# Kernel tuning notes

Measured on AMD Instinct MI355X. Metric: run time of the kernel, lower is better.

The kernel has to match this reference:

```python
import jax, jax.numpy as jnp
import numpy as np

NEG_SLOPE = 0.2  # PyG GATConv default negative_slope


def gat_conv(x, edge_index, W, a_src, a_dst, bias, heads, out_ch, concat):
    """PyG-style GATConv (eval mode, add_self_loops=True).
    x: [N, F_in], edge_index: [2, E] (row 0 = src, row 1 = dst).
    """
    N = x.shape[0]
    loop = jnp.arange(N, dtype=edge_index.dtype)
    src = jnp.concatenate([edge_index[0], loop])  # [E+N]
    dst = jnp.concatenate([edge_index[1], loop])

    h = (x @ W).reshape(N, heads, out_ch)            # [N, H, C]
    alpha_s = jnp.einsum('nhc,hc->nh', h, a_src)     # [N, H]
    alpha_d = jnp.einsum('nhc,hc->nh', h, a_dst)

    e = jax.nn.leaky_relu(alpha_s[src] + alpha_d[dst], NEG_SLOPE)  # [E+N, H]
    # softmax over incoming edges per destination node (numerically stable)
    m = jax.ops.segment_max(e, dst, num_segments=N)                # [N, H]
    ex = jnp.exp(e - m[dst])
    denom = jax.ops.segment_sum(ex, dst, num_segments=N)
    alpha = ex / (denom[dst] + 1e-16)                              # [E+N, H]

    msg = h[src] * alpha[:, :, None]                               # [E+N, H, C]
    out = jax.ops.segment_sum(msg, dst, num_segments=N)            # [N, H, C]
    out = out.reshape(N, heads * out_ch) if concat else out.mean(axis=1)
    return out + bias


def setup_inputs() -> dict:
    key = jax.random.key(0)
    ks = jax.random.split(key, 10)
    N, F_in, H, C1, LAT, E = 10000, 2000, 10, 128, 64, 150000
    hid = H * C1  # 1280
    x = jax.random.normal(ks[0], (N, F_in), dtype=jnp.float32)
    edge_index = jax.random.randint(ks[1], (2, E), 0, N, dtype=jnp.int64)
    # layer 1 params (glorot-ish scaling)
    W1 = jax.random.normal(ks[2], (F_in, H * C1), dtype=jnp.float32) * (1.0 / np.sqrt(F_in))
    a_src1 = jax.random.normal(ks[3], (H, C1), dtype=jnp.float32) * 0.1
    a_dst1 = jax.random.normal(ks[4], (H, C1), dtype=jnp.float32) * 0.1
    b1 = jnp.zeros((hid,), dtype=jnp.float32)
    # layer 2 params
    W2 = jax.random.normal(ks[5], (hid, H * LAT), dtype=jnp.float32) * (1.0 / np.sqrt(hid))
    a_src2 = jax.random.normal(ks[6], (H, LAT), dtype=jnp.float32) * 0.1
    a_dst2 = jax.random.normal(ks[7], (H, LAT), dtype=jnp.float32) * 0.1
    b2 = jnp.zeros((LAT,), dtype=jnp.float32)
    return {"x": x, "edge_index": edge_index,
            "W1": W1, "a_src1": a_src1, "a_dst1": a_dst1, "b1": b1,
            "W2": W2, "a_src2": a_src2, "a_dst2": a_dst2, "b2": b2}


def reference(x, edge_index, W1, a_src1, a_dst1, b1, W2, a_src2, a_dst2, b2):
    H, C1, LAT = 10, 128, 64
    h1 = gat_conv(x, edge_index, W1, a_src1, a_dst1, b1, H, C1, concat=True)
    h1 = jax.nn.relu(h1)
    h2 = gat_conv(h1, edge_index, W2, a_src2, a_dst2, b2, H, LAT, concat=False)
    return jax.nn.relu(h2)
```

## Files before the change

kernel.cpp:

```cpp
#include <hip/hip_runtime.h>

#define NN    10000
#define FIN   2000
#define NH    10
#define C1    128
#define C2    64
#define HC1   1280
#define HC2   640
#define MP    10240
#define K1P   2016

typedef _Float16 f16x8 __attribute__((ext_vector_type(8)));
typedef _Float16 f16x4 __attribute__((ext_vector_type(4)));
typedef _Float16 f16x2 __attribute__((ext_vector_type(2)));
typedef float    f32x4 __attribute__((ext_vector_type(4)));

__device__ __forceinline__ float leaky(float x) { return x > 0.f ? x : 0.2f * x; }

#define NCAST (2 * MP)
#define NW1   (63 * 40)
#define NW2   (40 * 20)
__global__ void k_prep(const float* __restrict__ x, _Float16* __restrict__ A1,
                       const float* __restrict__ W1, _Float16* __restrict__ W1t,
                       const float* __restrict__ W2, _Float16* __restrict__ W2t,
                       const int* __restrict__ ei, int* __restrict__ counts, int E) {
    __shared__ float tile[32][33];
    int bid = blockIdx.x, t = threadIdx.x;
    if (bid < NCAST) {
        int r = bid >> 1;
        int c = (bid & 1) * 256 + t;
        if (c >= K1P / 4) return;
        float4 v = make_float4(0.f, 0.f, 0.f, 0.f);
        if (r < NN && c < FIN / 4) v = *(const float4*)(x + (long)r * FIN + 4 * c);
        f16x4 o = {(_Float16)v.x, (_Float16)v.y, (_Float16)v.z, (_Float16)v.w};
        *(f16x4*)(A1 + (long)r * K1P + 4 * c) = o;
        return;
    }
    const float* W; _Float16* Wt; int K, N, Kpad, kbase, nbase;
    if (bid < NCAST + NW1) {
        int i = bid - NCAST;
        W = W1; Wt = W1t; K = FIN; N = HC1; Kpad = K1P;
        kbase = (i % 63) * 32; nbase = (i / 63) * 32;
    } else if (bid < NCAST + NW1 + NW2) {
        int i = bid - NCAST - NW1;
        W = W2; Wt = W2t; K = HC1; N = HC2; Kpad = HC1;
        kbase = (i % 40) * 32; nbase = (i / 40) * 32;
    } else {
        int e = (bid - NCAST - NW1 - NW2) * 256 + t;
        if (e < E) atomicAdd(&counts[ei[E + e]], 1);
        return;
    }
    int tx = t & 31, ty = t >> 5;
#pragma unroll
    for (int i = 0; i < 4; i++) {
        int k = kbase + ty + i * 8;
        float v = (k < K) ? W[(long)k * N + nbase + tx] : 0.0f;
        tile[ty + i * 8][tx] = v;
    }
    __syncthreads();
#pragma unroll
    for (int i = 0; i < 4; i++) {
        int n = nbase + ty + i * 8;
        Wt[(long)n * Kpad + kbase + tx] = (_Float16)tile[tx][ty + i * 8];
    }
}

__device__ __forceinline__ void gl2lds16(const void* g, void* l) {
    __builtin_amdgcn_global_load_lds((const __attribute__((address_space(1))) void*)g,
                                     (__attribute__((address_space(3))) void*)l, 16, 0, 0);
}

__global__ __launch_bounds__(512, 2) void k_gemm1(const _Float16* __restrict__ A,
                                                  const _Float16* __restrict__ Bt,
                                                  _Float16* __restrict__ C,
                                                  const float* __restrict__ asf,
                                                  const float* __restrict__ adf,
                                                  float* __restrict__ as,
                                                  float* __restrict__ ad,
                                                  int nblk,
                                                  const int* __restrict__ ei,
                                                  int* __restrict__ cursor,
                                                  int* __restrict__ colidx, int E) {
    constexpr int K    = K1P;
    constexpr int N    = HC1;
    constexpr int TBUF = 256 * 32;
    __shared__ char smem[3 * TBUF * 2 * 2] __attribute__((aligned(16)));
    _Float16* As = (_Float16*)smem;
    _Float16* Bs = (_Float16*)(smem + 3 * TBUF * 2);

    int bid = blockIdx.x;
    if (bid >= nblk) {
        int i = (bid - nblk) * 512 + threadIdx.x;
        if (i < E + NN) {
            int s, d;
            if (i < E) { s = ei[i]; d = ei[E + i]; }
            else       { s = i - E; d = i - E; }
            int pos = atomicAdd(&cursor[d], 1);
            colidx[pos] = s;
        }
        return;
    }
    int r = bid & 7, qb = bid >> 3;
    int n_t = qb % 5;
    int m_t = r + 8 * (qb / 5);
    int m0 = m_t * 256;
    int n0 = n_t * 256;
    int t = threadIdx.x;
    int lane = t & 63, wave = t >> 6;
    int wr = wave >> 2, wc = wave & 3;
    int lrow = lane & 15, q = lane >> 4;

    f32x4 acc[8][4] = {};

    int sS[2];
#pragma unroll
    for (int i = 0; i < 2; i++) sS[i] = t + 512 * i;
    const _Float16* Ar[2];
    const _Float16* Br[2];
#pragma unroll
    for (int i = 0; i < 2; i++) {
        int row = sS[i] >> 2, gq = (sS[i] & 3) ^ ((sS[i] >> 3) & 3);
        Ar[i] = A  + (long)(m0 + row) * K + gq * 8;
        Br[i] = Bt + (long)(n0 + row) * K + gq * 8;
    }

    int aoff[8], boff[4];
#pragma unroll
    for (int i = 0; i < 8; i++) {
        int rowa = wr * 128 + i * 16 + lrow;
        aoff[i] = rowa * 32 + ((q ^ ((rowa >> 1) & 3)) << 3);
    }
#pragma unroll
    for (int i = 0; i < 4; i++) {
        int rowb = wc * 64 + i * 16 + lrow;
        boff[i] = rowb * 32 + ((q ^ ((rowb >> 1) & 3)) << 3);
    }

    auto stage = [&](int it, int buf) {
        int k0 = it << 5;
#pragma unroll
        for (int i = 0; i < 2; i++) gl2lds16(Ar[i] + k0, &As[buf * TBUF + sS[i] * 8]);
#pragma unroll
        for (int i = 0; i < 2; i++) gl2lds16(Br[i] + k0, &Bs[buf * TBUF + sS[i] * 8]);
    };

    constexpr int WVM = 0x0F70 | 4;
    int nk = K >> 5;
    stage(0, 0);
    stage(1, 1);
    int cur = 0;
    for (int it = 0; it < nk; it++) {
        if (it + 1 < nk) __builtin_amdgcn_s_waitcnt(WVM);
        else             __builtin_amdgcn_s_waitcnt(0x0F70);
        __builtin_amdgcn_s_barrier();
        int nxt = cur + 2; if (nxt >= 3) nxt -= 3;
        if (it + 2 < nk) stage(it + 2, nxt);

        f16x8 af[8], bf[4];
#pragma unroll
        for (int i = 0; i < 8; i++) af[i] = *(const f16x8*)&As[cur * TBUF + aoff[i]];
#pragma unroll
        for (int i = 0; i < 4; i++) bf[i] = *(const f16x8*)&Bs[cur * TBUF + boff[i]];
#pragma unroll
        for (int mt = 0; mt < 8; mt++)
#pragma unroll
            for (int nt = 0; nt < 4; nt++)
                acc[mt][nt] = __builtin_amdgcn_mfma_f32_16x16x32_f16(bf[nt], af[mt], acc[mt][nt], 0, 0, 0);
        cur = (cur + 1 == 3) ? 0 : cur + 1;
    }

#pragma unroll
    for (int mt = 0; mt < 8; mt++) {
        int m = m0 + wr * 128 + mt * 16 + lrow;
#pragma unroll
        for (int nt = 0; nt < 4; nt++) {
            int n = n0 + wc * 64 + nt * 16 + q * 4;
            f16x4 o = {(_Float16)acc[mt][nt][0], (_Float16)acc[mt][nt][1],
                       (_Float16)acc[mt][nt][2], (_Float16)acc[mt][nt][3]};
            *(f16x4*)(C + (long)m * N + n) = o;
        }
    }

    float4 av[4], dvv[4];
#pragma unroll
    for (int nt = 0; nt < 4; nt++) {
        av[nt]  = *(const float4*)(asf + n0 + wc * 64 + nt * 16 + q * 4);
        dvv[nt] = *(const float4*)(adf + n0 + wc * 64 + nt * 16 + q * 4);
    }
    __syncthreads();
    float* sAs = (float*)smem;
    float* sAd = (float*)smem + 1024;
#pragma unroll
    for (int mt = 0; mt < 8; mt++) {
        float ps = 0.f, pd = 0.f;
#pragma unroll
        for (int nt = 0; nt < 4; nt++) {
            ps += acc[mt][nt][0] * av[nt].x + acc[mt][nt][1] * av[nt].y
                + acc[mt][nt][2] * av[nt].z + acc[mt][nt][3] * av[nt].w;
            pd += acc[mt][nt][0] * dvv[nt].x + acc[mt][nt][1] * dvv[nt].y
                + acc[mt][nt][2] * dvv[nt].z + acc[mt][nt][3] * dvv[nt].w;
        }
        ps += __shfl_xor(ps, 16); ps += __shfl_xor(ps, 32);
        pd += __shfl_xor(pd, 16); pd += __shfl_xor(pd, 32);
        if (q == 0) {
            int rl = wr * 128 + mt * 16 + lrow;
            sAs[rl * 4 + wc] = ps;
            sAd[rl * 4 + wc] = pd;
        }
    }
    __syncthreads();
    if (t < 256) {
        int m = m0 + t;
        if (m < NN) {
            int hb = n0 >> 7;
            as[m * NH + hb]     = sAs[t * 4 + 0] + sAs[t * 4 + 1];
            as[m * NH + hb + 1] = sAs[t * 4 + 2] + sAs[t * 4 + 3];
            ad[m * NH + hb]     = sAd[t * 4 + 0] + sAd[t * 4 + 1];
            ad[m * NH + hb + 1] = sAd[t * 4 + 2] + sAd[t * 4 + 3];
        }
    }
}

template<int MFRAG>
__global__ __launch_bounds__(256, 3) void k_gemm(const _Float16* __restrict__ A,
                                                 const _Float16* __restrict__ Bt,
                                                 _Float16* __restrict__ C, int K, int N,
                                                 int NTN,
                                                 const float* __restrict__ asf,
                                                 const float* __restrict__ adf,
                                                 float* __restrict__ as,
                                                 float* __restrict__ ad,
                                                 int headw, int nblk,
                                                 const int* __restrict__ ei,
                                                 int* __restrict__ cursor,
                                                 int* __restrict__ colidx, int E) {
    constexpr int BM   = MFRAG * 32;
    constexpr int ABUF = BM * 32;
    constexpr int ASL  = BM / 64;
    constexpr int WVM  = 0x0F70 | (ASL + 2);
    __shared__ char smem[3 * ABUF * 2 + 3 * 8192] __attribute__((aligned(16)));
    _Float16* As = (_Float16*)smem;
    _Float16* Bs = (_Float16*)(smem + 3 * ABUF * 2);

    int bid = blockIdx.x;
    if (bid >= nblk) {
        int i = (bid - nblk) * 256 + threadIdx.x;
        if (i < E + NN) {
            int s, d;
            if (i < E) { s = ei[i]; d = ei[E + i]; }
            else       { s = i - E; d = i - E; }
            int pos = atomicAdd(&cursor[d], 1);
            colidx[pos] = s;
        }
        return;
    }
    int r = bid & 7, qb = bid >> 3;
    int n_t = qb % NTN;
    int m_t = r + 8 * (qb / NTN);
    int m0 = m_t * BM;
    int n0 = n_t * 128;
    int t = threadIdx.x;
    int lane = t & 63, wave = t >> 6;
    int wr = wave >> 1, wc = wave & 1;
    int lrow = lane & 15, q = lane >> 4;

    f32x4 acc[MFRAG][4] = {};

    int sA[ASL], sB[2];
#pragma unroll
    for (int i = 0; i < ASL; i++) sA[i] = t + 256 * i;
#pragma unroll
    for (int i = 0; i < 2; i++) sB[i] = t + 256 * i;
    const _Float16* Ar[ASL];
    const _Float16* Br[2];
#pragma unroll
    for (int i = 0; i < ASL; i++) {
        int row = sA[i] >> 2, gq = (sA[i] & 3) ^ ((sA[i] >> 3) & 3);
        Ar[i] = A + (long)(m0 + row) * K + gq * 8;
    }
#pragma unroll
    for (int i = 0; i < 2; i++) {
        int row = sB[i] >> 2, gq = (sB[i] & 3) ^ ((sB[i] >> 3) & 3);
        Br[i] = Bt + (long)(n0 + row) * K + gq * 8;
    }

    int aoff[MFRAG], boff[4];
#pragma unroll
    for (int i = 0; i < MFRAG; i++) {
        int rowa = wr * (MFRAG * 16) + i * 16 + lrow;
        aoff[i] = rowa * 32 + ((q ^ ((rowa >> 1) & 3)) << 3);
    }
#pragma unroll
    for (int i = 0; i < 4; i++) {
        int rowb = wc * 64 + i * 16 + lrow;
        boff[i] = rowb * 32 + ((q ^ ((rowb >> 1) & 3)) << 3);
    }

    auto stage = [&](int it, int buf) {
        int k0 = it << 5;
#pragma unroll
        for (int i = 0; i < ASL; i++) gl2lds16(Ar[i] + k0, &As[buf * ABUF + sA[i] * 8]);
#pragma unroll
        for (int i = 0; i < 2; i++) gl2lds16(Br[i] + k0, &Bs[buf * 4096 + sB[i] * 8]);
    };

    int nk = K >> 5;
    stage(0, 0);
    stage(1, 1);
// ... 56 lines not shown
            sAs[rl * 2 + wc] = ps;
            sAd[rl * 2 + wc] = pd;
        }
    }
    __syncthreads();
    if (t < BM) {
        int m = m0 + t;
        if (m < NN) {
            int hb = n0 / headw;
            if (headw == 128) {
                as[m * NH + hb] = sAs[t * 2] + sAs[t * 2 + 1];
                ad[m * NH + hb] = sAd[t * 2] + sAd[t * 2 + 1];
            } else {
                as[m * NH + hb]     = sAs[t * 2];
                as[m * NH + hb + 1] = sAs[t * 2 + 1];
                ad[m * NH + hb]     = sAd[t * 2];
                ad[m * NH + hb + 1] = sAd[t * 2 + 1];
            }
        }
    }
}

__global__ void k_scan(const int* __restrict__ counts, int* rowptr, int* cursor, int n) {
    __shared__ int s[1024];
    int t = threadIdx.x;
    const int CH = (NN + 1023) / 1024;
    int base = t * CH;
    int loc[CH];
    int sum = 0;
#pragma unroll
    for (int i = 0; i < CH; i++) {
        int idx = base + i;
        int v = (idx < n) ? (counts[idx] + 1) : 0;
        loc[i] = sum;
        sum += v;
    }
    s[t] = sum;
    __syncthreads();
    for (int off = 1; off < 1024; off <<= 1) {
        int add = (t >= off) ? s[t - off] : 0;
        __syncthreads();
        s[t] += add;
        __syncthreads();
    }
    int pre = (t > 0) ? s[t - 1] : 0;
#pragma unroll
    for (int i = 0; i < CH; i++) {
        int idx = base + i;
        if (idx < n) { int ex = pre + loc[i]; rowptr[idx] = ex; cursor[idx] = ex; }
    }
    if (t == 1023) rowptr[n] = s[1023];
}

__global__ __launch_bounds__(320) void k_agg1(const int* __restrict__ rowptr,
                                              const int* __restrict__ colidx,
                                              const float* __restrict__ as,
                                              const float* __restrict__ ad,
                                              const _Float16* __restrict__ h,
                                              const float* __restrict__ bias,
                                              _Float16* __restrict__ A2) {
    __shared__ int sidx[64];
    __shared__ float sal[64 * NH];
    int n = blockIdx.x, t = threadIdx.x;
    if (n >= NN) {
        f16x4 z = {(_Float16)0.f, (_Float16)0.f, (_Float16)0.f, (_Float16)0.f};
        *(f16x4*)(A2 + (long)n * HC1 + 4 * t) = z;
        return;
    }
    int k0 = rowptr[n], deg = rowptr[n + 1] - k0;
    int w = t >> 6, lane = t & 63;
    int hd = t >> 5;
    float acc[4] = {0, 0, 0, 0};

    if (deg <= 64) {
        int src = (lane < deg) ? colidx[k0 + lane] : 0;
        float2 adv = *(const float2*)(ad + n * NH + 2 * w);
        float e0 = -1e30f, e1 = -1e30f;
        if (lane < deg) {
            float2 avv = *(const float2*)(as + (long)src * NH + 2 * w);
            e0 = leaky(avv.x + adv.x);
            e1 = leaky(avv.y + adv.y);
        }
        float m0 = e0, m1 = e1;
        for (int m = 32; m; m >>= 1) {
            m0 = fmaxf(m0, __shfl_xor(m0, m));
            m1 = fmaxf(m1, __shfl_xor(m1, m));
        }
        float x0 = (lane < deg) ? __expf(e0 - m0) : 0.f;
        float x1 = (lane < deg) ? __expf(e1 - m1) : 0.f;
        float s0 = x0, s1 = x1;
        for (int m = 32; m; m >>= 1) {
            s0 += __shfl_xor(s0, m);
            s1 += __shfl_xor(s1, m);
        }
        if (lane < deg) {
            sal[lane * NH + 2 * w]     = x0 / (s0 + 1e-16f);
            sal[lane * NH + 2 * w + 1] = x1 / (s1 + 1e-16f);
            if (w == 0) sidx[lane] = src;
        }
        __syncthreads();
        int j = 0;
        for (; j + 4 <= deg; j += 4) {
            int sj0 = sidx[j], sj1 = sidx[j + 1], sj2 = sidx[j + 2], sj3 = sidx[j + 3];
            float a0 = sal[j * NH + hd], a1 = sal[(j + 1) * NH + hd];
            float a2 = sal[(j + 2) * NH + hd], a3 = sal[(j + 3) * NH + hd];
            f16x4 v0 = *(const f16x4*)(h + (long)sj0 * HC1 + 4 * t);
            f16x4 v1 = *(const f16x4*)(h + (long)sj1 * HC1 + 4 * t);
            f16x4 v2 = *(const f16x4*)(h + (long)sj2 * HC1 + 4 * t);
            f16x4 v3 = *(const f16x4*)(h + (long)sj3 * HC1 + 4 * t);
#pragma unroll
            for (int i = 0; i < 4; i++)
                acc[i] += a0 * (float)v0[i] + a1 * (float)v1[i]
                        + a2 * (float)v2[i] + a3 * (float)v3[i];
        }
        for (; j < deg; j++) {
            int src2 = sidx[j];
            float a = sal[j * NH + hd];
            f16x4 v = *(const f16x4*)(h + (long)src2 * HC1 + 4 * t);
#pragma unroll
            for (int i = 0; i < 4; i++) acc[i] += a * (float)v[i];
        }
    } else {
        float2 adv = *(const float2*)(ad + n * NH + 2 * w);
        float m0 = -1e30f, m1 = -1e30f;
        for (int j = lane; j < deg; j += 64) {
            float2 avv = *(const float2*)(as + (long)colidx[k0 + j] * NH + 2 * w);
            m0 = fmaxf(m0, leaky(avv.x + adv.x));
            m1 = fmaxf(m1, leaky(avv.y + adv.y));
        }
        for (int m = 32; m; m >>= 1) {
            m0 = fmaxf(m0, __shfl_xor(m0, m));
            m1 = fmaxf(m1, __shfl_xor(m1, m));
        }
        float s0 = 0.f, s1 = 0.f;
        for (int j = lane; j < deg; j += 64) {
            float2 avv = *(const float2*)(as + (long)colidx[k0 + j] * NH + 2 * w);
            s0 += __expf(leaky(avv.x + adv.x) - m0);
            s1 += __expf(leaky(avv.y + adv.y) - m1);
        }
        for (int m = 32; m; m >>= 1) {
            s0 += __shfl_xor(s0, m);
            s1 += __shfl_xor(s1, m);
        }
        float i0 = 1.f / (s0 + 1e-16f), i1 = 1.f / (s1 + 1e-16f);
        for (int c0 = 0; c0 < deg; c0 += 64) {
            int cn = min(64, deg - c0);
            __syncthreads();
            if (lane < cn) {
                int src = colidx[k0 + c0 + lane];
                float2 avv = *(const float2*)(as + (long)src * NH + 2 * w);
                sal[lane * NH + 2 * w]     = __expf(leaky(avv.x + adv.x) - m0) * i0;
                sal[lane * NH + 2 * w + 1] = __expf(leaky(avv.y + adv.y) - m1) * i1;
                if (w == 0) sidx[lane] = src;
            }
            __syncthreads();
            for (int j = 0; j < cn; j++) {
                int src2 = sidx[j];
                float a = sal[j * NH + hd];
                f16x4 v = *(const f16x4*)(h + (long)src2 * HC1 + 4 * t);
#pragma unroll
                for (int i = 0; i < 4; i++) acc[i] += a * (float)v[i];
            }
        }
    }
    f16x4 o;
#pragma unroll
    for (int i = 0; i < 4; i++) {
        float x = acc[i] + bias[4 * t + i];
        o[i] = (_Float16)(x > 0.f ? x : 0.f);
    }
    *(f16x4*)(A2 + (long)n * HC1 + 4 * t) = o;
}

__global__ __launch_bounds__(320) void k_agg2(const int* __restrict__ rowptr,
                                              const int* __restrict__ colidx,
                                              const float* __restrict__ as,
                                              const float* __restrict__ ad,
                                              const _Float16* __restrict__ h,
                                              const float* __restrict__ bias,
                                              float* __restrict__ out) {
    __shared__ int sidx[64];
    __shared__ float sal[64 * NH];
    __shared__ float facc[HC2];
    int n = blockIdx.x, t = threadIdx.x;
    int k0 = rowptr[n], deg = rowptr[n + 1] - k0;
    int w = t >> 6, lane = t & 63;
    int hd = t >> 5;
    float a0 = 0.f, a1 = 0.f;

    if (deg <= 64) {
        int src = (lane < deg) ? colidx[k0 + lane] : 0;
        float2 adv = *(const float2*)(ad + n * NH + 2 * w);
        float e0 = -1e30f, e1 = -1e30f;
        if (lane < deg) {
            float2 avv = *(const float2*)(as + (long)src * NH + 2 * w);
            e0 = leaky(avv.x + adv.x);
            e1 = leaky(avv.y + adv.y);
        }
        float m0 = e0, m1 = e1;
        for (int m = 32; m; m >>= 1) {
            m0 = fmaxf(m0, __shfl_xor(m0, m));
            m1 = fmaxf(m1, __shfl_xor(m1, m));
        }
        float x0 = (lane < deg) ? __expf(e0 - m0) : 0.f;
        float x1 = (lane < deg) ? __expf(e1 - m1) : 0.f;
        float s0 = x0, s1 = x1;
        for (int m = 32; m; m >>= 1) {
            s0 += __shfl_xor(s0, m);
            s1 += __shfl_xor(s1, m);
        }
        if (lane < deg) {
            sal[lane * NH + 2 * w]     = x0 / (s0 + 1e-16f);
            sal[lane * NH + 2 * w + 1] = x1 / (s1 + 1e-16f);
            if (w == 0) sidx[lane] = src;
        }
        __syncthreads();
        int j = 0;
        for (; j + 4 <= deg; j += 4) {
            int sj0 = sidx[j], sj1 = sidx[j + 1], sj2 = sidx[j + 2], sj3 = sidx[j + 3];
            float b0 = sal[j * NH + hd], b1 = sal[(j + 1) * NH + hd];
            float b2 = sal[(j + 2) * NH + hd], b3 = sal[(j + 3) * NH + hd];
            f16x2 v0 = *(const f16x2*)(h + (long)sj0 * HC2 + 2 * t);
            f16x2 v1 = *(const f16x2*)(h + (long)sj1 * HC2 + 2 * t);
            f16x2 v2 = *(const f16x2*)(h + (long)sj2 * HC2 + 2 * t);
            f16x2 v3 = *(const f16x2*)(h + (long)sj3 * HC2 + 2 * t);
            a0 += b0 * (float)v0[0] + b1 * (float)v1[0] + b2 * (float)v2[0] + b3 * (float)v3[0];
            a1 += b0 * (float)v0[1] + b1 * (float)v1[1] + b2 * (float)v2[1] + b3 * (float)v3[1];
        }
        for (; j < deg; j++) {
            int src2 = sidx[j];
            float a = sal[j * NH + hd];
            f16x2 v = *(const f16x2*)(h + (long)src2 * HC2 + 2 * t);
            a0 += a * (float)v[0];
            a1 += a * (float)v[1];
        }
    } else {
        float2 adv = *(const float2*)(ad + n * NH + 2 * w);
        float m0 = -1e30f, m1 = -1e30f;
        for (int j = lane; j < deg; j += 64) {
            float2 avv = *(const float2*)(as + (long)colidx[k0 + j] * NH + 2 * w);
            m0 = fmaxf(m0, leaky(avv.x + adv.x));
            m1 = fmaxf(m1, leaky(avv.y + adv.y));
        }
        for (int m = 32; m; m >>= 1) {
            m0 = fmaxf(m0, __shfl_xor(m0, m));
            m1 = fmaxf(m1, __shfl_xor(m1, m));
        }
        float s0 = 0.f, s1 = 0.f;
        for (int j = lane; j < deg; j += 64) {
            float2 avv = *(const float2*)(as + (long)colidx[k0 + j] * NH + 2 * w);
            s0 += __expf(leaky(avv.x + adv.x) - m0);
            s1 += __expf(leaky(avv.y + adv.y) - m1);
        }
        for (int m = 32; m; m >>= 1) {
            s0 += __shfl_xor(s0, m);
            s1 += __shfl_xor(s1, m);
        }
        float i0 = 1.f / (s0 + 1e-16f), i1 = 1.f / (s1 + 1e-16f);
        for (int c0 = 0; c0 < deg; c0 += 64) {
            int cn = min(64, deg - c0);
            __syncthreads();
            if (lane < cn) {
                int src = colidx[k0 + c0 + lane];
                float2 avv = *(const float2*)(as + (long)src * NH + 2 * w);
                sal[lane * NH + 2 * w]     = __expf(leaky(avv.x + adv.x) - m0) * i0;
                sal[lane * NH + 2 * w + 1] = __expf(leaky(avv.y + adv.y) - m1) * i1;
                if (w == 0) sidx[lane] = src;
            }
            __syncthreads();
            for (int j = 0; j < cn; j++) {
                int src2 = sidx[j];
                float a = sal[j * NH + hd];
                f16x2 v = *(const f16x2*)(h + (long)src2 * HC2 + 2 * t);
                a0 += a * (float)v[0];
                a1 += a * (float)v[1];
            }
        }
    }
    facc[2 * t] = a0;
    facc[2 * t + 1] = a1;
    __syncthreads();
    if (t < C2) {
        float s = 0.f;
#pragma unroll
        for (int hh = 0; hh < NH; hh++) s += facc[hh * C2 + t];
        s = s * 0.1f + bias[t];
        out[(long)n * C2 + t] = s > 0.f ? s : 0.f;
    }
}

extern "C" void kernel_launch(void* const* d_in, const int* in_sizes, int n_in,
                              void* d_out, int out_size, void* d_ws, size_t ws_size,
                              hipStream_t stream) {
    const float* x      = (const float*)d_in[0];
    const int*   ei     = (const int*)d_in[1];
    const float* W1     = (const float*)d_in[2];
    const float* asrc1  = (const float*)d_in[3];
    const float* adst1  = (const float*)d_in[4];
    const float* b1     = (const float*)d_in[5];
    const float* W2     = (const float*)d_in[6];
    const float* asrc2  = (const float*)d_in[7];
    const float* adst2  = (const float*)d_in[8];
    const float* b2     = (const float*)d_in[9];
    float* out = (float*)d_out;
    const int E  = in_sizes[1] / 2;
    const int EN = E + NN;

    char* base = (char*)d_ws;
    size_t o = 0;
    auto alloc = [&](size_t bytes) { size_t r = o; o += (bytes + 255) & ~(size_t)255; return r; };
    _Float16* A1    = (_Float16*)(base + alloc((size_t)MP * K1P * 2));
    _Float16* W1t   = (_Float16*)(base + alloc((size_t)HC1 * K1P * 2));
    _Float16* A2    = (_Float16*)(base + alloc((size_t)MP * HC1 * 2));
    _Float16* W2t   = (_Float16*)(base + alloc((size_t)HC2 * HC1 * 2));
    _Float16* h1pre = (_Float16*)(base + alloc((size_t)MP * HC1 * 2));
    _Float16* h2pre = (_Float16*)(base + alloc((size_t)MP * HC2 * 2));
    float* as1      = (float*)(base + alloc((size_t)NN * NH * 4));
    float* ad1      = (float*)(base + alloc((size_t)NN * NH * 4));
    float* as2      = (float*)(base + alloc((size_t)NN * NH * 4));
    float* ad2      = (float*)(base + alloc((size_t)NN * NH * 4));
    int* counts     = (int*)(base + alloc((size_t)(NN + 1) * 4));
    int* rowptr     = (int*)(base + alloc((size_t)(NN + 1) * 4));
    int* cursor     = (int*)(base + alloc((size_t)(NN + 1) * 4));
    int* colidx     = (int*)(base + alloc((size_t)EN * 4));
    (void)ws_size; (void)n_in; (void)out_size;

    const int NCNT = (E + 255) / 256;
    const int FILLB = (EN + 511) / 512;
    const int G1 = 8 * (MP / 256 / 8) * (HC1 / 256);
    const int G2 = 8 * (MP / 128 / 8) * (HC2 / 128);

    hipMemsetAsync(counts, 0, (size_t)(NN + 1) * 4, stream);
    k_prep<<<NCAST + NW1 + NW2 + NCNT, 256, 0, stream>>>(x, A1, W1, W1t, W2, W2t, ei, counts, E);
    k_scan<<<1, 1024, 0, stream>>>(counts, rowptr, cursor, NN);
    k_gemm1<<<G1 + FILLB, 512, 0, stream>>>(A1, W1t, h1pre, asrc1, adst1, as1, ad1,
                                            G1, ei, cursor, colidx, E);
    k_agg1<<<MP, 320, 0, stream>>>(rowptr, colidx, as1, ad1, h1pre, b1, A2);
    k_gemm<4><<<G2, 256, 0, stream>>>(A2, W2t, h2pre, HC1, HC2, HC2 / 128,
                                      asrc2, adst2, as2, ad2, C2,
                                      G2, ei, cursor, colidx, E);
    k_agg2<<<NN, 320, 0, stream>>>(rowptr, colidx, as2, ad2, h2pre, b2, out);
}
```

Before: 359.1 us.

## Move CSR fill into prep kernel and split edge counting into own kernel

```diff
diff --git a/kernel.cpp b/kernel.cpp
--- a/kernel.cpp
+++ b/kernel.cpp
@@ -17,18 +17,36 @@
 
 __device__ __forceinline__ float leaky(float x) { return x > 0.f ? x : 0.2f * x; }
 
+__global__ void k_count(const int* __restrict__ ei, int* __restrict__ counts, int E) {
+    int e = blockIdx.x * 256 + threadIdx.x;
+    if (e < E) atomicAdd(&counts[ei[E + e]], 1);
+}
+
 #define NCAST (2 * MP)
 #define NW1   (63 * 40)
 #define NW2   (40 * 20)
 __global__ void k_prep(const float* __restrict__ x, _Float16* __restrict__ A1,
                        const float* __restrict__ W1, _Float16* __restrict__ W1t,
                        const float* __restrict__ W2, _Float16* __restrict__ W2t,
-                       const int* __restrict__ ei, int* __restrict__ counts, int E) {
+                       const int* __restrict__ ei, int* __restrict__ cursor,
+                       int* __restrict__ colidx, int E, int fillb) {
     __shared__ float tile[32][33];
     int bid = blockIdx.x, t = threadIdx.x;
-    if (bid < NCAST) {
-        int r = bid >> 1;
-        int c = (bid & 1) * 256 + t;
+    if (bid < fillb) {
+        int i = bid * 256 + t;
+        if (i < E + NN) {
+            int s, d;
+            if (i < E) { s = ei[i]; d = ei[E + i]; }
+            else       { s = i - E; d = i - E; }
+            int pos = atomicAdd(&cursor[d], 1);
+            colidx[pos] = s;
+        }
+        return;
+    }
+    int b = bid - fillb;
+    if (b < NCAST) {
+        int r = b >> 1;
+        int c = (b & 1) * 256 + t;
         if (c >= K1P / 4) return;
         float4 v = make_float4(0.f, 0.f, 0.f, 0.f);
         if (r < NN && c < FIN / 4) v = *(const float4*)(x + (long)r * FIN + 4 * c);
@@ -37,18 +55,14 @@
         return;
     }
     const float* W; _Float16* Wt; int K, N, Kpad, kbase, nbase;
-    if (bid < NCAST + NW1) {
-        int i = bid - NCAST;
+    if (b < NCAST + NW1) {
+        int i = b - NCAST;
         W = W1; Wt = W1t; K = FIN; N = HC1; Kpad = K1P;
         kbase = (i % 63) * 32; nbase = (i / 63) * 32;
-    } else if (bid < NCAST + NW1 + NW2) {
-        int i = bid - NCAST - NW1;
+    } else {
+        int i = b - NCAST - NW1;
         W = W2; Wt = W2t; K = HC1; N = HC2; Kpad = HC1;
         kbase = (i % 40) * 32; nbase = (i / 40) * 32;
-    } else {
-        int e = (bid - NCAST - NW1 - NW2) * 256 + t;
-        if (e < E) atomicAdd(&counts[ei[E + e]], 1);
-        return;
     }
     int tx = t & 31, ty = t >> 5;
 #pragma unroll
@@ -76,11 +90,7 @@
                                                   const float* __restrict__ asf,
                                                   const float* __restrict__ adf,
                                                   float* __restrict__ as,
-                                                  float* __restrict__ ad,
-                                                  int nblk,
-                                                  const int* __restrict__ ei,
-                                                  int* __restrict__ cursor,
-                                                  int* __restrict__ colidx, int E) {
+                                                  float* __restrict__ ad) {
     constexpr int K    = K1P;
     constexpr int N    = HC1;
     constexpr int TBUF = 256 * 32;
@@ -89,17 +99,6 @@
     _Float16* Bs = (_Float16*)(smem + 3 * TBUF * 2);
 
     int bid = blockIdx.x;
-    if (bid >= nblk) {
-        int i = (bid - nblk) * 512 + threadIdx.x;
-        if (i < E + NN) {
-            int s, d;
-            if (i < E) { s = ei[i]; d = ei[E + i]; }
-            else       { s = i - E; d = i - E; }
-            int pos = atomicAdd(&cursor[d], 1);
-            colidx[pos] = s;
-        }
-        return;
-    }
     int r = bid & 7, qb = bid >> 3;
     int n_t = qb % 5;
     int m_t = r + 8 * (qb / 5);
@@ -230,10 +229,7 @@
                                                  const float* __restrict__ adf,
                                                  float* __restrict__ as,
                                                  float* __restrict__ ad,
-                                                 int headw, int nblk,
-                                                 const int* __restrict__ ei,
-                                                 int* __restrict__ cursor,
-                                                 int* __restrict__ colidx, int E) {
+                                                 int headw) {
     constexpr int BM   = MFRAG * 32;
     constexpr int ABUF = BM * 32;
     constexpr int ASL  = BM / 64;
@@ -243,17 +239,6 @@
     _Float16* Bs = (_Float16*)(smem + 3 * ABUF * 2);
 
     int bid = blockIdx.x;
-    if (bid >= nblk) {
-        int i = (bid - nblk) * 256 + threadIdx.x;
-        if (i < E + NN) {
-            int s, d;
-            if (i < E) { s = ei[i]; d = ei[E + i]; }
-            else       { s = i - E; d = i - E; }
-            int pos = atomicAdd(&cursor[d], 1);
-            colidx[pos] = s;
-        }
-        return;
-    }
     int r = bid & 7, qb = bid >> 3;
     int n_t = qb % NTN;
     int m_t = r + 8 * (qb / NTN);
@@ -690,18 +675,18 @@
     (void)ws_size; (void)n_in; (void)out_size;
 
     const int NCNT = (E + 255) / 256;
-    const int FILLB = (EN + 511) / 512;
+    const int FILLB = (EN + 255) / 256;
     const int G1 = 8 * (MP / 256 / 8) * (HC1 / 256);
     const int G2 = 8 * (MP / 128 / 8) * (HC2 / 128);
 
     hipMemsetAsync(counts, 0, (size_t)(NN + 1) * 4, stream);
-    k_prep<<<NCAST + NW1 + NW2 + NCNT, 256, 0, stream>>>(x, A1, W1, W1t, W2, W2t, ei, counts, E);
+    k_count<<<NCNT, 256, 0, stream>>>(ei, counts, E);
     k_scan<<<1, 1024, 0, stream>>>(counts, rowptr, cursor, NN);
-    k_gemm1<<<G1 + FILLB, 512, 0, stream>>>(A1, W1t, h1pre, asrc1, adst1, as1, ad1,
-                                            G1, ei, cursor, colidx, E);
+    k_prep<<<FILLB + NCAST + NW1 + NW2, 256, 0, stream>>>(x, A1, W1, W1t, W2, W2t,
+                                                          ei, cursor, colidx, E, FILLB);
+    k_gemm1<<<G1, 512, 0, stream>>>(A1, W1t, h1pre, asrc1, adst1, as1, ad1);
     k_agg1<<<MP, 320, 0, stream>>>(rowptr, colidx, as1, ad1, h1pre, b1, A2);
     k_gemm<4><<<G2, 256, 0, stream>>>(A2, W2t, h2pre, HC1, HC2, HC2 / 128,
-                                      asrc2, adst2, as2, ad2, C2,
-                                      G2, ei, cursor, colidx, E);
+                                      asrc2, adst2, as2, ad2, C2);
     k_agg2<<<NN, 320, 0, stream>>>(rowptr, colidx, as2, ad2, h2pre, b2, out);
 }
```

Result: slower. 374.6 us (+4.3%).

## Restructure GAT aggregation to one wave per node-head using shuffles

Applied to the files above, without the earlier changes.

```diff
diff --git a/kernel.cpp b/kernel.cpp
--- a/kernel.cpp
+++ b/kernel.cpp
@@ -230,10 +230,7 @@
                                                  const float* __restrict__ adf,
                                                  float* __restrict__ as,
                                                  float* __restrict__ ad,
-                                                 int headw, int nblk,
-                                                 const int* __restrict__ ei,
-                                                 int* __restrict__ cursor,
-                                                 int* __restrict__ colidx, int E) {
+                                                 int headw) {
     constexpr int BM   = MFRAG * 32;
     constexpr int ABUF = BM * 32;
     constexpr int ASL  = BM / 64;
@@ -243,17 +240,6 @@
     _Float16* Bs = (_Float16*)(smem + 3 * ABUF * 2);
 
     int bid = blockIdx.x;
-    if (bid >= nblk) {
-        int i = (bid - nblk) * 256 + threadIdx.x;
-        if (i < E + NN) {
-            int s, d;
-            if (i < E) { s = ei[i]; d = ei[E + i]; }
-            else       { s = i - E; d = i - E; }
-            int pos = atomicAdd(&cursor[d], 1);
-            colidx[pos] = s;
-        }
-        return;
-    }
     int r = bid & 7, qb = bid >> 3;
     int n_t = qb % NTN;
     int m_t = r + 8 * (qb / NTN);
@@ -416,240 +402,181 @@
     if (t == 1023) rowptr[n] = s[1023];
 }
 
-__global__ __launch_bounds__(320) void k_agg1(const int* __restrict__ rowptr,
+__global__ __launch_bounds__(256) void k_agg1(const int* __restrict__ rowptr,
                                               const int* __restrict__ colidx,
                                               const float* __restrict__ as,
                                               const float* __restrict__ ad,
                                               const _Float16* __restrict__ h,
                                               const float* __restrict__ bias,
                                               _Float16* __restrict__ A2) {
-    __shared__ int sidx[64];
-    __shared__ float sal[64 * NH];
-    int n = blockIdx.x, t = threadIdx.x;
+    int bid = blockIdx.x;
+    int head = bid / (MP / 4);
+    int ng   = bid % (MP / 4);
+    int wave = threadIdx.x >> 6, lane = threadIdx.x & 63;
+    int n = ng * 4 + wave;
+    int cb = head * C1 + 2 * lane;
     if (n >= NN) {
-        f16x4 z = {(_Float16)0.f, (_Float16)0.f, (_Float16)0.f, (_Float16)0.f};
-        *(f16x4*)(A2 + (long)n * HC1 + 4 * t) = z;
+        f16x2 z = {(_Float16)0.f, (_Float16)0.f};
+        *(f16x2*)(A2 + (long)n * HC1 + cb) = z;
         return;
     }
     int k0 = rowptr[n], deg = rowptr[n + 1] - k0;
-    int w = t >> 6, lane = t & 63;
-    int hd = t >> 5;
-    float acc[4] = {0, 0, 0, 0};
+    float adv = ad[n * NH + head];
+    float a0 = 0.f, a1 = 0.f;
 
     if (deg <= 64) {
         int src = (lane < deg) ? colidx[k0 + lane] : 0;
-        float2 adv = *(const float2*)(ad + n * NH + 2 * w);
-        float e0 = -1e30f, e1 = -1e30f;
-        if (lane < deg) {
-            float2 avv = *(const float2*)(as + (long)src * NH + 2 * w);
-            e0 = leaky(avv.x + adv.x);
-            e1 = leaky(avv.y + adv.y);
-        }
-        float m0 = e0, m1 = e1;
-        for (int m = 32; m; m >>= 1) {
-            m0 = fmaxf(m0, __shfl_xor(m0, m));
-            m1 = fmaxf(m1, __shfl_xor(m1, m));
-        }
-        float x0 = (lane < deg) ? __expf(e0 - m0) : 0.f;
-        float x1 = (lane < deg) ? __expf(e1 - m1) : 0.f;
-        float s0 = x0, s1 = x1;
-        for (int m = 32; m; m >>= 1) {
-            s0 += __shfl_xor(s0, m);
-            s1 += __shfl_xor(s1, m);
-        }
-        if (lane < deg) {
-            sal[lane * NH + 2 * w]     = x0 / (s0 + 1e-16f);
-            sal[lane * NH + 2 * w + 1] = x1 / (s1 + 1e-16f);
-            if (w == 0) sidx[lane] = src;
-        }
-        __syncthreads();
+        float e = (lane < deg) ? leaky(as[(long)src * NH + head] + adv) : -1e30f;
+        float m = e;
+        for (int mm = 32; mm; mm >>= 1) m = fmaxf(m, __shfl_xor(m, mm));
+        float x = (lane < deg) ? __expf(e - m) : 0.f;
+        float s = x;
+        for (int mm = 32; mm; mm >>= 1) s += __shfl_xor(s, mm);
+        float alp = x / (s + 1e-16f);
         int j = 0;
         for (; j + 4 <= deg; j += 4) {
-            int sj0 = sidx[j], sj1 = sidx[j + 1], sj2 = sidx[j + 2], sj3 = sidx[j + 3];
-            float a0 = sal[j * NH + hd], a1 = sal[(j + 1) * NH + hd];
-            float a2 = sal[(j + 2) * NH + hd], a3 = sal[(j + 3) * NH + hd];
-            f16x4 v0 = *(const f16x4*)(h + (long)sj0 * HC1 + 4 * t);
-            f16x4 v1 = *(const f16x4*)(h + (long)sj1 * HC1 + 4 * t);
-            f16x4 v2 = *(const f16x4*)(h + (long)sj2 * HC1 + 4 * t);
-            f16x4 v3 = *(const f16x4*)(h + (long)sj3 * HC1 + 4 * t);
-#pragma unroll
-            for (int i = 0; i < 4; i++)
-                acc[i] += a0 * (float)v0[i] + a1 * (float)v1[i]
-                        + a2 * (float)v2[i] + a3 * (float)v3[i];
+            int s0 = __shfl(src, j),     s1 = __shfl(src, j + 1);
+            int s2 = __shfl(src, j + 2), s3 = __shfl(src, j + 3);
+            float b0 = __shfl(alp, j),     b1 = __shfl(alp, j + 1);
+            float b2 = __shfl(alp, j + 2), b3 = __shfl(alp, j + 3);
+            f16x2 v0 = *(const f16x2*)(h + (long)s0 * HC1 + cb);
+            f16x2 v1 = *(const f16x2*)(h + (long)s1 * HC1 + cb);
+            f16x2 v2 = *(const f16x2*)(h + (long)s2 * HC1 + cb);
+            f16x2 v3 = *(const f16x2*)(h + (long)s3 * HC1 + cb);
+            a0 += b0 * (float)v0[0] + b1 * (float)v1[0] + b2 * (float)v2[0] + b3 * (float)v3[0];
+            a1 += b0 * (float)v0[1] + b1 * (float)v1[1] + b2 * (float)v2[1] + b3 * (float)v3[1];
         }
         for (; j < deg; j++) {
-            int src2 = sidx[j];
-            float a = sal[j * NH + hd];
-            f16x4 v = *(const f16x4*)(h + (long)src2 * HC1 + 4 * t);
-#pragma unroll
-            for (int i = 0; i < 4; i++) acc[i] += a * (float)v[i];
+            int sj = __shfl(src, j);
+            float bj = __shfl(alp, j);
+            f16x2 v = *(const f16x2*)(h + (long)sj * HC1 + cb);
+            a0 += bj * (float)v[0];
+            a1 += bj * (float)v[1];
         }
     } else {
-        float2 adv = *(const float2*)(ad + n * NH + 2 * w);
-        float m0 = -1e30f, m1 = -1e30f;
-        for (int j = lane; j < deg; j += 64) {
-            float2 avv = *(const float2*)(as + (long)colidx[k0 + j] * NH + 2 * w);
-            m0 = fmaxf(m0, leaky(avv.x + adv.x));
-            m1 = fmaxf(m1, leaky(avv.y + adv.y));
-        }
-        for (int m = 32; m; m >>= 1) {
-            m0 = fmaxf(m0, __shfl_xor(m0, m));
-            m1 = fmaxf(m1, __shfl_xor(m1, m));
-        }
-        float s0 = 0.f, s1 = 0.f;
-        for (int j = lane; j < deg; j += 64) {
-            float2 avv = *(const float2*)(as + (long)colidx[k0 + j] * NH + 2 * w);
-            s0 += __expf(leaky(avv.x + adv.x) - m0);
-            s1 += __expf(leaky(avv.y + adv.y) - m1);
-        }
-        for (int m = 32; m; m >>= 1) {
-            s0 += __shfl_xor(s0, m);
-            s1 += __shfl_xor(s1, m);
-        }
-        float i0 = 1.f / (s0 + 1e-16f), i1 = 1.f / (s1 + 1e-16f);
+        float m = -1e30f;
+        for (int j2 = lane; j2 < deg; j2 += 64)
+            m = fmaxf(m, leaky(as[(long)colidx[k0 + j2] * NH + head] + adv));
+        for (int mm = 32; mm; mm >>= 1) m = fmaxf(m, __shfl_xor(m, mm));
+        float s = 0.f;
+        for (int j2 = lane; j2 < deg; j2 += 64)
+            s += __expf(leaky(as[(long)colidx[k0 + j2] * NH + head] + adv) - m);
+        for (int mm = 32; mm; mm >>= 1) s += __shfl_xor(s, mm);
+        float inv = 1.f / (s + 1e-16f);
         for (int c0 = 0; c0 < deg; c0 += 64) {
             int cn = min(64, deg - c0);
-            __syncthreads();
-            if (lane < cn) {
-                int src = colidx[k0 + c0 + lane];
-                float2 avv = *(const float2*)(as + (long)src * NH + 2 * w);
-                sal[lane * NH + 2 * w]     = __expf(leaky(avv.x + adv.x) - m0) * i0;
-                sal[lane * NH + 2 * w + 1] = __expf(leaky(avv.y + adv.y) - m1) * i1;
-                if (w == 0) sidx[lane] = src;
+            int src = (lane < cn) ? colidx[k0 + c0 + lane] : 0;
+            float alp = (lane < cn)
+                ? __expf(leaky(as[(long)src * NH + head] + adv) - m) * inv : 0.f;
+            int j = 0;
+            for (; j + 4 <= cn; j += 4) {
+                int s0 = __shfl(src, j),     s1 = __shfl(src, j + 1);
+                int s2 = __shfl(src, j + 2), s3 = __shfl(src, j + 3);
+                float b0 = __shfl(alp, j),     b1 = __shfl(alp, j + 1);
+                float b2 = __shfl(alp, j + 2), b3 = __shfl(alp, j + 3);
+                f16x2 v0 = *(const f16x2*)(h + (long)s0 * HC1 + cb);
+                f16x2 v1 = *(const f16x2*)(h + (long)s1 * HC1 + cb);
+                f16x2 v2 = *(const f16x2*)(h + (long)s2 * HC1 + cb);
+                f16x2 v3 = *(const f16x2*)(h + (long)s3 * HC1 + cb);
+                a0 += b0 * (float)v0[0] + b1 * (float)v1[0] + b2 * (float)v2[0] + b3 * (float)v3[0];
+                a1 += b0 * (float)v0[1] + b1 * (float)v1[1] + b2 * (float)v2[1] + b3 * (float)v3[1];
             }
-            __syncthreads();
-            for (int j = 0; j < cn; j++) {
-                int src2 = sidx[j];
-                float a = sal[j * NH + hd];
-                f16x4 v = *(const f16x4*)(h + (long)src2 * HC1 + 4 * t);
-#pragma unroll
-                for (int i = 0; i < 4; i++) acc[i] += a * (float)v[i];
+            for (; j < cn; j++) {
+                int sj = __shfl(src, j);
+                float bj = __shfl(alp, j);
+                f16x2 v = *(const f16x2*)(h + (long)sj * HC1 + cb);
+                a0 += bj * (float)v[0];
+                a1 += bj * (float)v[1];
             }
         }
     }
-    f16x4 o;
-#pragma unroll
-    for (int i = 0; i < 4; i++) {
-        float x = acc[i] + bias[4 * t + i];
-        o[i] = (_Float16)(x > 0.f ? x : 0.f);
-    }
-    *(f16x4*)(A2 + (long)n * HC1 + 4 * t) = o;
-}
-
-__global__ __launch_bounds__(320) void k_agg2(const int* __restrict__ rowptr,
+    float xb0 = a0 + bias[cb], xb1 = a1 + bias[cb + 1];
+    f16x2 o = {(_Float16)(xb0 > 0.f ? xb0 : 0.f), (_Float16)(xb1 > 0.f ? xb1 : 0.f)};
+    *(f16x2*)(A2 + (long)n * HC1 + cb) = o;
+}
+
+__global__ __launch_bounds__(256) void k_agg2(const int* __restrict__ rowptr,
                                               const int* __restrict__ colidx,
                                               const float* __restrict__ as,
                                               const float* __restrict__ ad,
                                               const _Float16* __restrict__ h,
-                                              const float* __restrict__ bias,
-                                              float* __restrict__ out) {
-    __shared__ int sidx[64];
-    __shared__ float sal[64 * NH];
-    __shared__ float facc[HC2];
-    int n = blockIdx.x, t = threadIdx.x;
+                                              float* __restrict__ tacc) {
+    int bid = blockIdx.x;
+    int head = bid / (NN / 4);
+    int ng   = bid % (NN / 4);
+    int wave = threadIdx.x >> 6, lane = threadIdx.x & 63;
+    int n = ng * 4 + wave;
     int k0 = rowptr[n], deg = rowptr[n + 1] - k0;
-    int w = t >> 6, lane = t & 63;
-    int hd = t >> 5;
-    float a0 = 0.f, a1 = 0.f;
+    float adv = ad[n * NH + head];
+    const _Float16* hh = h + head * C2 + lane;
+    float a = 0.f;
 
     if (deg <= 64) {
         int src = (lane < deg) ? colidx[k0 + lane] : 0;
-        float2 adv = *(const float2*)(ad + n * NH + 2 * w);
-        float e0 = -1e30f, e1 = -1e30f;
-        if (lane < deg) {
-            float2 avv = *(const float2*)(as + (long)src * NH + 2 * w);
-            e0 = leaky(avv.x + adv.x);
-            e1 = leaky(avv.y + adv.y);
-        }
-        float m0 = e0, m1 = e1;
-        for (int m = 32; m; m >>= 1) {
-            m0 = fmaxf(m0, __shfl_xor(m0, m));
-            m1 = fmaxf(m1, __shfl_xor(m1, m));
-        }
-        float x0 = (lane < deg) ? __expf(e0 - m0) : 0.f;
-        float x1 = (lane < deg) ? __expf(e1 - m1) : 0.f;
-        float s0 = x0, s1 = x1;
-        for (int m = 32; m; m >>= 1) {
-            s0 += __shfl_xor(s0, m);
-            s1 += __shfl_xor(s1, m);
-        }
-        if (lane < deg) {
-            sal[lane * NH + 2 * w]     = x0 / (s0 + 1e-16f);
-            sal[lane * NH + 2 * w + 1] = x1 / (s1 + 1e-16f);
-            if (w == 0) sidx[lane] = src;
-        }
-        __syncthreads();
+        float e = (lane < deg) ? leaky(as[(long)src * NH + head] + adv) : -1e30f;
+        float m = e;
+        for (int mm = 32; mm; mm >>= 1) m = fmaxf(m, __shfl_xor(m, mm));
+        float x = (lane < deg) ? __expf(e - m) : 0.f;
+        float s = x;
+        for (int mm = 32; mm; mm >>= 1) s += __shfl_xor(s, mm);
+        float alp = x / (s + 1e-16f);
         int j = 0;
         for (; j + 4 <= deg; j += 4) {
-            int sj0 = sidx[j], sj1 = sidx[j + 1], sj2 = sidx[j + 2], sj3 = sidx[j + 3];
-            float b0 = sal[j * NH + hd], b1 = sal[(j + 1) * NH + hd];
-            float b2 = sal[(j + 2) * NH + hd], b3 = sal[(j + 3) * NH + hd];
-            f16x2 v0 = *(const f16x2*)(h + (long)sj0 * HC2 + 2 * t);
-            f16x2 v1 = *(const f16x2*)(h + (long)sj1 * HC2 + 2 * t);
-            f16x2 v2 = *(const f16x2*)(h + (long)sj2 * HC2 + 2 * t);
-            f16x2 v3 = *(const f16x2*)(h + (long)sj3 * HC2 + 2 * t);
-            a0 += b0 * (float)v0[0] + b1 * (float)v1[0] + b2 * (float)v2[0] + b3 * (float)v3[0];
-            a1 += b0 * (float)v0[1] + b1 * (float)v1[1] + b2 * (float)v2[1] + b3 * (float)v3[1];
+            int s0 = __shfl(src, j),     s1 = __shfl(src, j + 1);
+            int s2 = __shfl(src, j + 2), s3 = __shfl(src, j + 3);
+            float b0 = __shfl(alp, j),     b1 = __shfl(alp, j + 1);
+            float b2 = __shfl(alp, j + 2), b3 = __shfl(alp, j + 3);
+            float v0 = (float)hh[(long)s0 * HC2];
+            float v1 = (float)hh[(long)s1 * HC2];
+            float v2 = (float)hh[(long)s2 * HC2];
+            float v3 = (float)hh[(long)s3 * HC2];
+            a += b0 * v0 + b1 * v1 + b2 * v2 + b3 * v3;
         }
         for (; j < deg; j++) {
-            int src2 = sidx[j];
-            float a = sal[j * NH + hd];
-            f16x2 v = *(const f16x2*)(h + (long)src2 * HC2 + 2 * t);
-            a0 += a * (float)v[0];
-            a1 += a * (float)v[1];
+            int sj = __shfl(src, j);
+            float bj = __shfl(alp, j);
+            a += bj * (float)hh[(long)sj * HC2];
         }
     } else {
-        float2 adv = *(const float2*)(ad + n * NH + 2 * w);
-        float m0 = -1e30f, m1 = -1e30f;
-        for (int j = lane; j < deg; j += 64) {
-            float2 avv = *(const float2*)(as + (long)colidx[k0 + j] * NH + 2 * w);
-            m0 = fmaxf(m0, leaky(avv.x + adv.x));
-            m1 = fmaxf(m1, leaky(avv.y + adv.y));
-        }
-        for (int m = 32; m; m >>= 1) {
-            m0 = fmaxf(m0, __shfl_xor(m0, m));
-            m1 = fmaxf(m1, __shfl_xor(m1, m));
-        }
-        float s0 = 0.f, s1 = 0.f;
-        for (int j = lane; j < deg; j += 64) {
-            float2 avv = *(const float2*)(as + (long)colidx[k0 + j] * NH + 2 * w);
-            s0 += __expf(leaky(avv.x + adv.x) - m0);
-            s1 += __expf(leaky(avv.y + adv.y) - m1);
-        }
-        for (int m = 32; m; m >>= 1) {
-            s0 += __shfl_xor(s0, m);
-            s1 += __shfl_xor(s1, m);
-        }
-        float i0 = 1.f / (s0 + 1e-16f), i1 = 1.f / (s1 + 1e-16f);
+        float m = -1e30f;
+        for (int j2 = lane; j2 < deg; j2 += 64)
+            m = fmaxf(m, leaky(as[(long)colidx[k0 + j2] * NH + head] + adv));
+        for (int mm = 32; mm; mm >>= 1) m = fmaxf(m, __shfl_xor(m, mm));
+        float s = 0.f;
+        for (int j2 = lane; j2 < deg; j2 += 64)
+            s += __expf(leaky(as[(long)colidx[k0 + j2] * NH + head] + adv) - m);
+        for (int mm = 32; mm; mm >>= 1) s += __shfl_xor(s, mm);
+        float inv = 1.f / (s + 1e-16f);
         for (int c0 = 0; c0 < deg; c0 += 64) {
             int cn = min(64, deg - c0);
-            __syncthreads();
-            if (lane < cn) {
-                int src = colidx[k0 + c0 + lane];
-                float2 avv = *(const float2*)(as + (long)src * NH + 2 * w);
-                sal[lane * NH + 2 * w]     = __expf(leaky(avv.x + adv.x) - m0) * i0;
-                sal[lane * NH + 2 * w + 1] = __expf(leaky(avv.y + adv.y) - m1) * i1;
-                if (w == 0) sidx[lane] = src;
+            int src = (lane < cn) ? colidx[k0 + c0 + lane] : 0;
+            float alp = (lane < cn)
+                ? __expf(leaky(as[(long)src * NH + head] + adv) - m) * inv : 0.f;
+            int j = 0;
+            for (; j + 4 <= cn; j += 4) {
+                int s0 = __shfl(src, j),     s1 = __shfl(src, j + 1);
+                int s2 = __shfl(src, j + 2), s3 = __shfl(src, j + 3);
+                float b0 = __shfl(alp, j),     b1 = __shfl(alp, j + 1);
+                float b2 = __shfl(alp, j + 2), b3 = __shfl(alp, j + 3);
+                a += b0 * (float)hh[(long)s0 * HC2] + b1 * (float)hh[(long)s1 * HC2]
+                   + b2 * (float)hh[(long)s2 * HC2] + b3 * (float)hh[(long)s3 * HC2];
             }
-            __syncthreads();
-            for (int j = 0; j < cn; j++) {
-                int src2 = sidx[j];
-                float a = sal[j * NH + hd];
-                f16x2 v = *(const f16x2*)(h + (long)src2 * HC2 + 2 * t);
-                a0 += a * (float)v[0];
-                a1 += a * (float)v[1];
+            for (; j < cn; j++) {
+                int sj = __shfl(src, j);
+                float bj = __shfl(alp, j);
+                a += bj * (float)hh[(long)sj * HC2];
             }
         }
     }
-    facc[2 * t] = a0;
-    facc[2 * t + 1] = a1;
-    __syncthreads();
-    if (t < C2) {
-        float s = 0.f;
-#pragma unroll
-        for (int hh = 0; hh < NH; hh++) s += facc[hh * C2 + t];
-        s = s * 0.1f + bias[t];
-        out[(long)n * C2 + t] = s > 0.f ? s : 0.f;
+    atomicAdd(&tacc[n * C2 + lane], a);
+}
+
+__global__ void k_fin(const float* __restrict__ tacc, const float* __restrict__ bias,
+                      float* __restrict__ out) {
+    int i = blockIdx.x * 256 + threadIdx.x;
+    if (i < NN * C2) {
+        float s = tacc[i] * 0.1f + bias[i & (C2 - 1)];
+        out[i] = s > 0.f ? s : 0.f;
     }
 }
 
@@ -683,6 +610,7 @@
     float* ad1      = (float*)(base + alloc((size_t)NN * NH * 4));
     float* as2      = (float*)(base + alloc((size_t)NN * NH * 4));
     float* ad2      = (float*)(base + alloc((size_t)NN * NH * 4));
+    float* tacc     = (float*)(base + alloc((size_t)NN * C2 * 4));
     int* counts     = (int*)(base + alloc((size_t)(NN + 1) * 4));
     int* rowptr     = (int*)(base + alloc((size_t)(NN + 1) * 4));
     int* cursor     = (int*)(base + alloc((size_t)(NN + 1) * 4));
@@ -695,13 +623,14 @@
     const int G2 = 8 * (MP / 128 / 8) * (HC2 / 128);
 
     hipMemsetAsync(counts, 0, (size_t)(NN + 1) * 4, stream);
+    hipMemsetAsync(tacc, 0, (size_t)NN * C2 * 4, stream);
     k_prep<<<NCAST + NW1 + NW2 + NCNT, 256, 0, stream>>>(x, A1, W1, W1t, W2, W2t, ei, counts, E);
     k_scan<<<1, 1024, 0, stream>>>(counts, rowptr, cursor, NN);
     k_gemm1<<<G1 + FILLB, 512, 0, stream>>>(A1, W1t, h1pre, asrc1, adst1, as1, ad1,
                                             G1, ei, cursor, colidx, E);
-    k_agg1<<<MP, 320, 0, stream>>>(rowptr, colidx, as1, ad1, h1pre, b1, A2);
+    k_agg1<<<NH * (MP / 4), 256, 0, stream>>>(rowptr, colidx, as1, ad1, h1pre, b1, A2);
     k_gemm<4><<<G2, 256, 0, stream>>>(A2, W2t, h2pre, HC1, HC2, HC2 / 128,
-                                      asrc2, adst2, as2, ad2, C2,
-                                      G2, ei, cursor, colidx, E);
-    k_agg2<<<NN, 320, 0, stream>>>(rowptr, colidx, as2, ad2, h2pre, b2, out);
-}
+                                      asrc2, adst2, as2, ad2, C2);
+    k_agg2<<<NH * (NN / 4), 256, 0, stream>>>(rowptr, colidx, as2, ad2, h2pre, tacc);
+    k_fin<<<(NN * C2 + 255) / 256, 256, 0, stream>>>(tacc, b2, out);
+}
```

Result: slower. 382.0 us (+6.4%).

## Split GEMM1 K-loop across two sequential launches and enlarge GEMM2 tiles

Applied to the files above, without the earlier changes.

```diff
diff --git a/kernel.cpp b/kernel.cpp
--- a/kernel.cpp
+++ b/kernel.cpp
@@ -73,10 +73,12 @@
 __global__ __launch_bounds__(512, 2) void k_gemm1(const _Float16* __restrict__ A,
                                                   const _Float16* __restrict__ Bt,
                                                   _Float16* __restrict__ C,
+                                                  float* __restrict__ Cpart,
                                                   const float* __restrict__ asf,
                                                   const float* __restrict__ adf,
                                                   float* __restrict__ as,
                                                   float* __restrict__ ad,
+                                                  int kstart, int ksteps, int final_,
                                                   int nblk,
                                                   const int* __restrict__ ei,
                                                   int* __restrict__ cursor,
@@ -120,8 +122,8 @@
 #pragma unroll
     for (int i = 0; i < 2; i++) {
         int row = sS[i] >> 2, gq = (sS[i] & 3) ^ ((sS[i] >> 3) & 3);
-        Ar[i] = A  + (long)(m0 + row) * K + gq * 8;
-        Br[i] = Bt + (long)(n0 + row) * K + gq * 8;
+        Ar[i] = A  + (long)(m0 + row) * K + gq * 8 + kstart;
+        Br[i] = Bt + (long)(n0 + row) * K + gq * 8 + kstart;
     }
 
     int aoff[8], boff[4];
@@ -145,16 +147,15 @@
     };
 
     constexpr int WVM = 0x0F70 | 4;
-    int nk = K >> 5;
     stage(0, 0);
     stage(1, 1);
     int cur = 0;
-    for (int it = 0; it < nk; it++) {
-        if (it + 1 < nk) __builtin_amdgcn_s_waitcnt(WVM);
-        else             __builtin_amdgcn_s_waitcnt(0x0F70);
+    for (int it = 0; it < ksteps; it++) {
+        if (it + 1 < ksteps) __builtin_amdgcn_s_waitcnt(WVM);
+        else                 __builtin_amdgcn_s_waitcnt(0x0F70);
         __builtin_amdgcn_s_barrier();
         int nxt = cur + 2; if (nxt >= 3) nxt -= 3;
-        if (it + 2 < nk) stage(it + 2, nxt);
+        if (it + 2 < ksteps) stage(it + 2, nxt);
 
         f16x8 af[8], bf[4];
 #pragma unroll
@@ -167,6 +168,30 @@
             for (int nt = 0; nt < 4; nt++)
                 acc[mt][nt] = __builtin_amdgcn_mfma_f32_16x16x32_f16(bf[nt], af[mt], acc[mt][nt], 0, 0, 0);
         cur = (cur + 1 == 3) ? 0 : cur + 1;
+    }
+
+    if (!final_) {
+#pragma unroll
+        for (int mt = 0; mt < 8; mt++) {
+            int m = m0 + wr * 128 + mt * 16 + lrow;
+#pragma unroll
+            for (int nt = 0; nt < 4; nt++) {
+                int n = n0 + wc * 64 + nt * 16 + q * 4;
+                *(f32x4*)(Cpart + (long)m * N + n) = acc[mt][nt];
+            }
+        }
+        return;
+    }
+#pragma unroll
+    for (int mt = 0; mt < 8; mt++) {
+        int m = m0 + wr * 128 + mt * 16 + lrow;
+#pragma unroll
+        for (int nt = 0; nt < 4; nt++) {
+            int n = n0 + wc * 64 + nt * 16 + q * 4;
+            f32x4 p = *(const f32x4*)(Cpart + (long)m * N + n);
+#pragma unroll
+            for (int i = 0; i < 4; i++) acc[mt][nt][i] += p[i];
+        }
     }
 
 #pragma unroll
@@ -230,10 +255,7 @@
                                                  const float* __restrict__ adf,
                                                  float* __restrict__ as,
                                                  float* __restrict__ ad,
-                                                 int headw, int nblk,
-                                                 const int* __restrict__ ei,
-                                                 int* __restrict__ cursor,
-                                                 int* __restrict__ colidx, int E) {
+                                                 int headw) {
     constexpr int BM   = MFRAG * 32;
     constexpr int ABUF = BM * 32;
     constexpr int ASL  = BM / 64;
@@ -243,17 +265,6 @@
     _Float16* Bs = (_Float16*)(smem + 3 * ABUF * 2);
 
     int bid = blockIdx.x;
-    if (bid >= nblk) {
-        int i = (bid - nblk) * 256 + threadIdx.x;
-        if (i < E + NN) {
-            int s, d;
-            if (i < E) { s = ei[i]; d = ei[E + i]; }
-            else       { s = i - E; d = i - E; }
-            int pos = atomicAdd(&cursor[d], 1);
-            colidx[pos] = s;
-        }
-        return;
-    }
     int r = bid & 7, qb = bid >> 3;
     int n_t = qb % NTN;
     int m_t = r + 8 * (qb / NTN);
@@ -687,21 +698,23 @@
     int* rowptr     = (int*)(base + alloc((size_t)(NN + 1) * 4));
     int* cursor     = (int*)(base + alloc((size_t)(NN + 1) * 4));
     int* colidx     = (int*)(base + alloc((size_t)EN * 4));
+    float* Cpart    = (float*)(base + alloc((size_t)MP * HC1 * 4));
     (void)ws_size; (void)n_in; (void)out_size;
 
     const int NCNT = (E + 255) / 256;
     const int FILLB = (EN + 511) / 512;
     const int G1 = 8 * (MP / 256 / 8) * (HC1 / 256);
-    const int G2 = 8 * (MP / 128 / 8) * (HC2 / 128);
+    const int G2 = 8 * (MP / 256 / 8) * (HC2 / 128);
 
     hipMemsetAsync(counts, 0, (size_t)(NN + 1) * 4, stream);
     k_prep<<<NCAST + NW1 + NW2 + NCNT, 256, 0, stream>>>(x, A1, W1, W1t, W2, W2t, ei, counts, E);
     k_scan<<<1, 1024, 0, stream>>>(counts, rowptr, cursor, NN);
-    k_gemm1<<<G1 + FILLB, 512, 0, stream>>>(A1, W1t, h1pre, asrc1, adst1, as1, ad1,
-                                            G1, ei, cursor, colidx, E);
+    k_gemm1<<<G1 + FILLB, 512, 0, stream>>>(A1, W1t, h1pre, Cpart, asrc1, adst1, as1, ad1,
+                                            0, 31, 0, G1, ei, cursor, colidx, E);
+    k_gemm1<<<G1, 512, 0, stream>>>(A1, W1t, h1pre, Cpart, asrc1, adst1, as1, ad1,
+                                    992, 32, 1, G1, ei, cursor, colidx, E);
     k_agg1<<<MP, 320, 0, stream>>>(rowptr, colidx, as1, ad1, h1pre, b1, A2);
-    k_gemm<4><<<G2, 256, 0, stream>>>(A2, W2t, h2pre, HC1, HC2, HC2 / 128,
-                                      asrc2, adst2, as2, ad2, C2,
-                                      G2, ei, cursor, colidx, E);
+    k_gemm<8><<<G2, 256, 0, stream>>>(A2, W2t, h2pre, HC1, HC2, HC2 / 128,
+                                      asrc2, adst2, as2, ad2, C2);
     k_agg2<<<NN, 320, 0, stream>>>(rowptr, colidx, as2, ad2, h2pre, b2, out);
 }
```

Result: slower. 395.4 us (+10.1%).
